# Kernel optimization log

Measured on AMD Instinct MI355X. Metric: run time of the kernel, lower is better.

## Reference

```python
import jax, jax.numpy as jnp
import numpy as np

B, N, E, FIMG = 8, 10242, 61440, 512


def setup_inputs() -> dict:
    key = jax.random.key(0)
    ks = jax.random.split(key, 16)
    inp = {
        "batch_vertices": jax.random.normal(ks[0], (B, N, 3), jnp.float32),
        "img_features": jax.random.normal(ks[1], (B, FIMG), jnp.float32),
        "edge_indices": jax.random.randint(ks[2], (2, E), 0, N, dtype=jnp.int32),
    }
    dims = [(3 + FIMG, 512), (512, 512), (512, 512), (512, 512), (512, 64), (64, 3)]
    for i, (fi, fo) in enumerate(dims, 1):
        inp[f"W{i}"] = jax.random.normal(ks[2 + i], (fi, fo), jnp.float32) / np.sqrt(fi).astype(np.float32)
        inp[f"b{i}"] = jnp.zeros((fo,), jnp.float32)
    return inp


def _gcn(x, W, b, src, dst, norm, n):
    # GCNConv: h = x @ W ; out[i] = sum_{(j->i)} norm_e * h[j] ; + b
    h = jnp.einsum('bnf,fo->bno', x, W)
    msg = h[:, src, :] * norm[None, :, None]        # [B, E+N, Fo]
    out = jnp.zeros((x.shape[0], n, W.shape[1]), x.dtype).at[:, dst, :].add(msg)
    return out + b


def reference(batch_vertices, img_features, edge_indices,
              W1, b1, W2, b2, W3, b3, W4, b4, W5, b5, W6, b6):
    n = batch_vertices.shape[1]
    loop = jnp.arange(n, dtype=edge_indices.dtype)
    src = jnp.concatenate([edge_indices[0], loop])  # add self-loops (GCN)
    dst = jnp.concatenate([edge_indices[1], loop])
    deg = jnp.zeros((n,), jnp.float32).at[dst].add(1.0)
    dinv = jnp.where(deg > 0, jax.lax.rsqrt(deg), 0.0)
    norm = dinv[src] * dinv[dst]                    # symmetric normalization

    feat = jnp.broadcast_to(img_features[:, None, :], (batch_vertices.shape[0], n, img_features.shape[1]))
    x = jnp.concatenate([batch_vertices, feat], axis=2)

    x = _gcn(x, W1, b1, src, dst, norm, n)
    x = _gcn(x, W2, b2, src, dst, norm, n)
    x = jax.nn.relu(x)
    x = _gcn(x, W3, b3, src, dst, norm, n)
    x = _gcn(x, W4, b4, src, dst, norm, n)
    x = jax.nn.relu(x)
    x = _gcn(x, W5, b5, src, dst, norm, n)
    x = _gcn(x, W6, b6, src, dst, norm, n)
    return x
```

## Files before the change

kernel.cpp:

```cpp
#include <hip/hip_runtime.h>
#include <hip/hip_bf16.h>

typedef __attribute__((ext_vector_type(8))) short short8_t;
typedef __attribute__((ext_vector_type(4))) float f32x4;

#define DEV __device__ __forceinline__

constexpr int BB = 8;
constexpr int NV = 10242;
constexpr int NE = 61440;
constexpr int MROWS = BB * NV;
constexpr int KD = 512;

DEV float bf2f(ushort u) { union { unsigned i; float f; } v; v.i = ((unsigned)u) << 16; return v.f; }
DEV ushort f2bf(float f) {
    union { unsigned i; float f; } v; v.f = f;
    unsigned b = v.i;
    b += 0x7fffu + ((b >> 16) & 1u);
    return (ushort)(b >> 16);
}

__global__ void k_init(int* deg, int* fill) {
    int i = blockIdx.x * 256 + threadIdx.x;
    if (i < NV) { deg[i] = 1; fill[i] = 0; }
}

__global__ void k_count(const int* __restrict__ ei, int* __restrict__ deg) {
    int e = blockIdx.x * 256 + threadIdx.x;
    if (e < NE) atomicAdd(&deg[ei[NE + e]], 1);
}

__global__ __launch_bounds__(1024) void k_scan(const int* __restrict__ cnt, int* __restrict__ rp) {
    __shared__ int part[1024];
    const int t = threadIdx.x;
    const int chunk = (NV + 1023) / 1024;
    int b0 = t * chunk, b1 = min(b0 + chunk, NV);
    int s = 0;
    for (int i = b0; i < b1; ++i) s += cnt[i];
    part[t] = s;
    __syncthreads();
    for (int off = 1; off < 1024; off <<= 1) {
        int v = (t >= off) ? part[t - off] : 0;
        __syncthreads();
        part[t] += v;
        __syncthreads();
    }
    int run = (t == 0) ? 0 : part[t - 1];
    for (int i = b0; i < b1; ++i) { rp[i] = run; run += cnt[i]; }
    if (t == 1023) rp[NV] = part[1023];
}

__global__ void k_fill(const int* __restrict__ ei, const int* __restrict__ rp,
                       int* __restrict__ fill, const int* __restrict__ deg,
                       int* __restrict__ ci, float* __restrict__ val) {
    int e = blockIdx.x * 256 + threadIdx.x;
    if (e >= NE + NV) return;
    int s, d;
    if (e < NE) { s = ei[e]; d = ei[NE + e]; }
    else        { s = d = e - NE; }
    int p = atomicAdd(&fill[d], 1);
    int pos = rp[d] + p;
    ci[pos] = s;
    val[pos] = rsqrtf((float)deg[s]) * rsqrtf((float)deg[d]);
}

__global__ void k_srow(const int* __restrict__ rp, const float* __restrict__ val, float* __restrict__ s) {
    int i = blockIdx.x * 256 + threadIdx.x;
    if (i >= NV) return;
    float a = 0.f;
    for (int e = rp[i]; e < rp[i + 1]; ++e) a += val[e];
    s[i] = a;
}

__global__ void k_s2(const int* __restrict__ rp, const int* __restrict__ ci,
                     const float* __restrict__ val, const float* __restrict__ s, float* __restrict__ s2) {
    int i = blockIdx.x * 256 + threadIdx.x;
    if (i >= NV) return;
    float a = 0.f;
    for (int e = rp[i]; e < rp[i + 1]; ++e) a += val[e] * s[ci[e]];
    s2[i] = a;
}

__global__ __launch_bounds__(256) void k_aggsm(const float* __restrict__ src, float* __restrict__ dst,
                                               const int* __restrict__ rp, const int* __restrict__ ci,
                                               const float* __restrict__ val) {
    int idx = blockIdx.x * 256 + threadIdx.x;
    if (idx >= MROWS) return;
    int b = idx / NV, i = idx - b * NV;
    float a0 = 0.f, a1 = 0.f, a2 = 0.f;
    const float* sb = src + (size_t)b * NV * 3;
    for (int e = rp[i]; e < rp[i + 1]; ++e) {
        int j = ci[e];
        float wv = val[e];
        a0 = fmaf(wv, sb[j * 3 + 0], a0);
        a1 = fmaf(wv, sb[j * 3 + 1], a1);
        a2 = fmaf(wv, sb[j * 3 + 2], a2);
    }
    float* o = dst + ((size_t)b * NV + i) * 3;
    o[0] = a0; o[1] = a1; o[2] = a2;
}

__global__ void k_wprep(const float* __restrict__ W4, const float* __restrict__ W3,
                        const float* __restrict__ W5, ushort* __restrict__ Wt4,
                        ushort* __restrict__ W3c, ushort* __restrict__ Wt5) {
    int idx = blockIdx.x * 256 + threadIdx.x;
    if (idx < 512 * 512) {
        int n = idx >> 9, k = idx & 511;
        Wt4[idx] = f2bf(W4[k * 512 + n]);
    } else if (idx < 2 * 512 * 512) {
        int j = idx - 512 * 512;
        W3c[j] = f2bf(W3[j]);
    } else {
        int j = idx - 2 * 512 * 512;
        if (j < 64 * 512) {
            int n = j >> 9, k = j & 511;
            Wt5[j] = f2bf(W5[k * 64 + n]);
        }
    }
}

__global__ __launch_bounds__(128) void k_small1(const float* __restrict__ W1, const float* __restrict__ b1,
                                                const float* __restrict__ b3, const float* __restrict__ W2,
                                                const float* __restrict__ W4, float* __restrict__ CW12,
                                                float* __restrict__ b1w2, float* __restrict__ b3w4) {
    int c = blockIdx.x * 128 + threadIdx.x;
    int y = blockIdx.y;
    const float* Mrow = (y < 3) ? (W1 + y * 512) : (y == 3 ? b1 : b3);
    const float* W = (y < 4) ? W2 : W4;
    float a = 0.f;
    for (int k = 0; k < 512; ++k) a = fmaf(Mrow[k], W[(size_t)k * 512 + c], a);
    float* o = (y < 3) ? (CW12 + y * 512) : (y == 3 ? b1w2 : b3w4);
    o[c] = a;
}

__global__ __launch_bounds__(128) void k_l1base(const float* __restrict__ img, const float* __restrict__ W1,
                                                float* __restrict__ base) {
    int c = blockIdx.x * 128 + threadIdx.x;
    int b = blockIdx.y;
    float s = 0.f;
    for (int k = 0; k < 512; ++k) s = fmaf(img[b * 512 + k], W1[(size_t)(3 + k) * 512 + c], s);
    base[b * 512 + c] = s;
}

__global__ __launch_bounds__(128) void k_matvecs(const float* __restrict__ M, const float* __restrict__ W,
                                                 float* __restrict__ out) {
    int c = blockIdx.x * 128 + threadIdx.x;
    int r = blockIdx.y;
    float a = 0.f;
    for (int k = 0; k < 512; ++k) a = fmaf(M[r * 512 + k], W[(size_t)k * 512 + c], a);
    out[r * 512 + c] = a;
}

__global__ __launch_bounds__(256) void k_x2(const float* __restrict__ aggV2, const float* __restrict__ s,
                                            const float* __restrict__ s2, const float* __restrict__ CW12,
                                            const float* __restrict__ bw2, const float* __restrict__ b1w2,
                                            const float* __restrict__ b2, ushort* __restrict__ r2) {
    const int t = threadIdx.x;
    int row = blockIdx.x * 2 + (t >> 7);
    if (row >= MROWS) return;
    int i = row >> 3, b = row & 7;
    const float* av = aggV2 + ((size_t)b * NV + i) * 3;
    float a0 = av[0], a1 = av[1], a2 = av[2];
    float si = s[i], s2i = s2[i];
    int c = (t & 127) * 4;
    float4 w0 = *(const float4*)&CW12[c];
    float4 w1 = *(const float4*)&CW12[512 + c];
    float4 w2 = *(const float4*)&CW12[1024 + c];
    float4 bw = *(const float4*)&bw2[b * 512 + c];
    float4 bv = *(const float4*)&b1w2[c];
    float4 b2v = *(const float4*)&b2[c];
    float o0 = a0 * w0.x + a1 * w1.x + a2 * w2.x + s2i * bw.x + si * bv.x + b2v.x;
    float o1 = a0 * w0.y + a1 * w1.y + a2 * w2.y + s2i * bw.y + si * bv.y + b2v.y;
    float o2 = a0 * w0.z + a1 * w1.z + a2 * w2.z + s2i * bw.z + si * bv.z + b2v.z;
    float o3 = a0 * w0.w + a1 * w1.w + a2 * w2.w + s2i * bw.w + si * bv.w + b2v.w;
    ushort4 o;
    o.x = f2bf(fmaxf(o0, 0.f));
    o.y = f2bf(fmaxf(o1, 0.f));
    o.z = f2bf(fmaxf(o2, 0.f));
    o.w = f2bf(fmaxf(o3, 0.f));
    *(ushort4*)&r2[(size_t)row * 512 + c] = o;
}

template <int EPI>
__global__ __launch_bounds__(256) void k_gemm(const ushort* __restrict__ A, const ushort* __restrict__ Bt,
                                              ushort* __restrict__ C, int Mr, int Nc,
                                              const float* __restrict__ sv, const float* __restrict__ eb1,
                                              const float* __restrict__ eb2) {
    const int ncb = (Nc + 127) >> 7;
    const int nrc = (Mr + 127) >> 7;
    const int cpx = (nrc + 7) >> 3;
    const int bid = blockIdx.x;
    const int xcd = bid & 7;
    const int k = bid >> 3;
    const int rc = xcd * cpx + k / ncb;
    const int cb = k % ncb;
    if (rc >= nrc) return;

    __shared__ __align__(16) ushort lA[2][4096];
    __shared__ __align__(16) ushort lB[2][4096];
    const int t = threadIdx.x;
    const int lane = t & 63, w = t >> 6;
    const int wr = w >> 1, wc = w & 1;
    const int r0 = rc * 128, c0 = cb * 128;

    const ushort* gA[2]; const ushort* gB[2];
    int ldsoff[2];
    #pragma unroll
    for (int i2 = 0; i2 < 2; ++i2) {
        int idx = i2 * 256 + t;
        int row = idx >> 2, slot = idx & 3;
        int srcslot = slot ^ ((row >> 1) & 3);
        int ar = min(r0 + row, Mr - 1);
        int bc = min(c0 + row, Nc - 1);
        gA[i2] = A + (size_t)ar * KD + srcslot * 8;
        gB[i2] = Bt + (size_t)bc * KD + srcslot * 8;
        ldsoff[i2] = idx * 8;
    }

    auto stage = [&](int buf, int kt) {
        int ko = kt * 32;
        #pragma unroll
        for (int i2 = 0; i2 < 2; ++i2) {
            __builtin_amdgcn_global_load_lds(
                (const __attribute__((address_space(1))) void*)(gA[i2] + ko),
                (__attribute__((address_space(3))) void*)(&lA[buf][ldsoff[i2]]), 16, 0, 0);
            __builtin_amdgcn_global_load_lds(
                (const __attribute__((address_space(1))) void*)(gB[i2] + ko),
                (__attribute__((address_space(3))) void*)(&lB[buf][ldsoff[i2]]), 16, 0, 0);
        }
    };

    f32x4 acc[4][4] = {};
    stage(0, 0);
    __syncthreads();
    int cur = 0;
    const int rloc = lane & 15;
    const int kb = lane >> 4;
    const int kbs = (kb ^ ((rloc >> 1) & 3)) * 8;
    for (int kt = 0; kt < 16; ++kt) {
        if (kt < 15) stage(cur ^ 1, kt + 1);
        short8_t af[4], bfr[4];
        #pragma unroll
        for (int m = 0; m < 4; ++m) {
            af[m]  = *(const short8_t*)&lA[cur][(wr * 64 + m * 16 + rloc) * 32 + kbs];
            bfr[m] = *(const short8_t*)&lB[cur][(wc * 64 + m * 16 + rloc) * 32 + kbs];
        }
        #pragma unroll
        for (int m = 0; m < 4; ++m)
            #pragma unroll
            for (int n = 0; n < 4; ++n)
                acc[m][n] = __builtin_amdgcn_mfma_f32_16x16x32_bf16(bfr[n], af[m], acc[m][n], 0, 0, 0);
        __syncthreads();
        cur ^= 1;
    }

    #pragma unroll
    for (int m = 0; m < 4; ++m) {
        const int gr = r0 + wr * 64 + m * 16 + rloc;
        if (gr >= Mr) continue;
        #pragma unroll
        for (int n = 0; n < 4; ++n) {
            const int qc = c0 + wc * 64 + n * 16;
            if (qc >= Nc) continue;
            const int gc = qc + kb * 4;
            float v0 = acc[m][n][0], v1 = acc[m][n][1], v2 = acc[m][n][2], v3 = acc[m][n][3];
            if (EPI == 1) {
                const float s = sv[gr >> 3];
                const float4 e1 = *(const float4*)&eb1[gc];
                const float4 e2 = *(const float4*)&eb2[gc];
                v0 = fmaxf(v0 + s * e1.x + e2.x, 0.f);
                v1 = fmaxf(v1 + s * e1.y + e2.y, 0.f);
                v2 = fmaxf(v2 + s * e1.z + e2.z, 0.f);
                v3 = fmaxf(v3 + s * e1.w + e2.w, 0.f);
            }
            ushort4 o;
            o.x = f2bf(v0); o.y = f2bf(v1); o.z = f2bf(v2); o.w = f2bf(v3);
            *(ushort4*)&C[(size_t)gr * Nc + gc] = o;
        }
    }
}

__global__ __launch_bounds__(256) void k_gemm64(const ushort* __restrict__ A, const ushort* __restrict__ Bt,
                                                ushort* __restrict__ C) {
    const int rc = blockIdx.x;
    const int r0 = rc * 256;
    __shared__ __align__(16) ushort lA[2][8192];
    __shared__ __align__(16) ushort lB[2][2048];
    const int t = threadIdx.x;
    const int lane = t & 63, w = t >> 6;

    const ushort* gA[4]; int loffA[4];
    #pragma unroll
    for (int p = 0; p < 4; ++p) {
        int idx = p * 256 + t;
        int row = idx >> 2, slot = idx & 3;
        int srcslot = slot ^ ((row >> 1) & 3);
        int ar = min(r0 + row, MROWS - 1);
        gA[p] = A + (size_t)ar * KD + srcslot * 8;
        loffA[p] = idx * 8;
    }
    const int brow = t >> 2, bslot = (t & 3) ^ ((brow >> 1) & 3);
    const ushort* gB = Bt + (size_t)brow * KD + bslot * 8;
    const int loffB = t * 8;

    auto stage = [&](int buf, int kt) {
        int ko = kt * 32;
        #pragma unroll
        for (int p = 0; p < 4; ++p)
            __builtin_amdgcn_global_load_lds(
                (const __attribute__((address_space(1))) void*)(gA[p] + ko),
                (__attribute__((address_space(3))) void*)(&lA[buf][loffA[p]]), 16, 0, 0);
        __builtin_amdgcn_global_load_lds(
            (const __attribute__((address_space(1))) void*)(gB + ko),
            (__attribute__((address_space(3))) void*)(&lB[buf][loffB]), 16, 0, 0);
    };

    f32x4 acc[4][4] = {};
    stage(0, 0);
    __syncthreads();
    int cur = 0;
    const int rloc = lane & 15;
    const int kb = lane >> 4;
    const int kbs = (kb ^ ((rloc >> 1) & 3)) * 8;
    for (int kt = 0; kt < 16; ++kt) {
        if (kt < 15) stage(cur ^ 1, kt + 1);
        short8_t af[4], bfr[4];
        #pragma unroll
        for (int m = 0; m < 4; ++m) {
            af[m]  = *(const short8_t*)&lA[cur][(w * 64 + m * 16 + rloc) * 32 + kbs];
            bfr[m] = *(const short8_t*)&lB[cur][(m * 16 + rloc) * 32 + kbs];
        }
        #pragma unroll
        for (int m = 0; m < 4; ++m)
            #pragma unroll
            for (int n = 0; n < 4; ++n)
                acc[m][n] = __builtin_amdgcn_mfma_f32_16x16x32_bf16(bfr[n], af[m], acc[m][n], 0, 0, 0);
        __syncthreads();
        cur ^= 1;
    }

    #pragma unroll
    for (int m = 0; m < 4; ++m) {
        const int gr = r0 + w * 64 + m * 16 + rloc;
        if (gr >= MROWS) continue;
        #pragma unroll
        for (int n = 0; n < 4; ++n) {
            const int gc = n * 16 + kb * 4;
            ushort4 o;
            o.x = f2bf(acc[m][n][0]); o.y = f2bf(acc[m][n][1]);
            o.z = f2bf(acc[m][n][2]); o.w = f2bf(acc[m][n][3]);
            *(ushort4*)&C[(size_t)gr * 64 + gc] = o;
        }
    }
}

template <bool RELU>
__global__ __launch_bounds__(512) void k_aggv(const ushort* __restrict__ h, ushort* __restrict__ xo,
                                              const int* __restrict__ rp, const int* __restrict__ ci,
                                              const float* __restrict__ val) {
    constexpr int CH = BB * 512;
    const int i = blockIdx.x;
    const int t = threadIdx.x;
    const int r0 = rp[i], r1 = rp[i + 1];
    const ushort* hb = h + t * 8;
    float acc[8] = {};
    for (int e = r0; e < r1; e += 4) {
        const bool p1 = e + 1 < r1, p2 = e + 2 < r1, p3 = e + 3 < r1;
        const int j0 = ci[e];
        const int j1 = p1 ? ci[e + 1] : j0;
        const int j2 = p2 ? ci[e + 2] : j0;
        const int j3 = p3 ? ci[e + 3] : j0;
        const float w0 = val[e];
        const float w1 = p1 ? val[e + 1] : 0.f;
        const float w2 = p2 ? val[e + 2] : 0.f;
        const float w3 = p3 ? val[e + 3] : 0.f;
        const short8_t v0 = *(const short8_t*)(hb + (size_t)j0 * CH);
        const short8_t v1 = *(const short8_t*)(hb + (size_t)j1 * CH);
        const short8_t v2 = *(const short8_t*)(hb + (size_t)j2 * CH);
        const short8_t v3 = *(const short8_t*)(hb + (size_t)j3 * CH);
        #pragma unroll
        for (int k = 0; k < 8; ++k) {
            float a = acc[k];
            a = fmaf(w0, bf2f((ushort)v0[k]), a);
            a = fmaf(w1, bf2f((ushort)v1[k]), a);
            a = fmaf(w2, bf2f((ushort)v2[k]), a);
            a = fmaf(w3, bf2f((ushort)v3[k]), a);
            acc[k] = a;
        }
    }
    short8_t o;
    #pragma unroll
    for (int k = 0; k < 8; ++k) {
        float a = acc[k];
        if (RELU) a = fmaxf(a, 0.f);
        o[k] = (short)f2bf(a);
    }
    *(short8_t*)(xo + (size_t)i * CH + t * 8) = o;
}

__global__ __launch_bounds__(64) void k_aggv64f(const ushort* __restrict__ h, float* __restrict__ h3,
                                                const int* __restrict__ rp, const int* __restrict__ ci,
                                                const float* __restrict__ val, const float* __restrict__ b5,
                                                const float* __restrict__ W6) {
    constexpr int CH = BB * 64;
    __shared__ float w6[192];
    const int t = threadIdx.x;
    w6[t] = W6[t]; w6[t + 64] = W6[t + 64]; w6[t + 128] = W6[t + 128];
    __syncthreads();
    const int i = blockIdx.x;
    const int r0 = rp[i], r1 = rp[i + 1];
    const ushort* hb = h + t * 8;
    float acc[8] = {};
    for (int e = r0; e < r1; e += 4) {
        const bool p1 = e + 1 < r1, p2 = e + 2 < r1, p3 = e + 3 < r1;
        const int j0 = ci[e];
        const int j1 = p1 ? ci[e + 1] : j0;
        const int j2 = p2 ? ci[e + 2] : j0;
        const int j3 = p3 ? ci[e + 3] : j0;
        const float w0 = val[e];
        const float w1 = p1 ? val[e + 1] : 0.f;
        const float w2 = p2 ? val[e + 2] : 0.f;
        const float w3 = p3 ? val[e + 3] : 0.f;
        const short8_t v0 = *(const short8_t*)(hb + (size_t)j0 * CH);
        const short8_t v1 = *(const short8_t*)(hb + (size_t)j1 * CH);
        const short8_t v2 = *(const short8_t*)(hb + (size_t)j2 * CH);
        const short8_t v3 = *(const short8_t*)(hb + (size_t)j3 * CH);
        #pragma unroll
        for (int k = 0; k < 8; ++k) {
            float a = acc[k];
            a = fmaf(w0, bf2f((ushort)v0[k]), a);
            a = fmaf(w1, bf2f((ushort)v1[k]), a);
            a = fmaf(w2, bf2f((ushort)v2[k]), a);
            a = fmaf(w3, bf2f((ushort)v3[k]), a);
            acc[k] = a;
        }
    }
    const int fb = (t & 7) * 8;
    float p0 = 0.f, p1 = 0.f, p2 = 0.f;
    #pragma unroll
    for (int k = 0; k < 8; ++k) {
        float a = acc[k] + b5[fb + k];
        p0 = fmaf(a, w6[(fb + k) * 3 + 0], p0);
        p1 = fmaf(a, w6[(fb + k) * 3 + 1], p1);
        p2 = fmaf(a, w6[(fb + k) * 3 + 2], p2);
    }
    p0 += __shfl_xor(p0, 1); p0 += __shfl_xor(p0, 2); p0 += __shfl_xor(p0, 4);
    p1 += __shfl_xor(p1, 1); p1 += __shfl_xor(p1, 2); p1 += __shfl_xor(p1, 4);
    p2 += __shfl_xor(p2, 1); p2 += __shfl_xor(p2, 2); p2 += __shfl_xor(p2, 4);
    if ((t & 7) == 0) {
        int row = i * 8 + (t >> 3);
        float* o = h3 + (size_t)row * 3;
        o[0] = p0; o[1] = p1; o[2] = p2;
    }
}

__global__ __launch_bounds__(256) void k_agg3(const float* __restrict__ h3, float* __restrict__ out,
                                              const int* __restrict__ rp, const int* __restrict__ ci,
                                              const float* __restrict__ val, const float* __restrict__ b6) {
    int idx = blockIdx.x * 256 + threadIdx.x;
    if (idx >= MROWS) return;
    int b = idx / NV, i = idx - b * NV;
    float a0 = b6[0], a1 = b6[1], a2 = b6[2];
    int r0 = rp[i], r1 = rp[i + 1];
    for (int e = r0; e < r1; ++e) {
        int j = ci[e];
        float wv = val[e];
        const float* hr = h3 + ((size_t)j * BB + b) * 3;
        a0 = fmaf(wv, hr[0], a0);
        a1 = fmaf(wv, hr[1], a1);
        a2 = fmaf(wv, hr[2], a2);
    }
    float* o = out + (size_t)idx * 3;
    o[0] = a0; o[1] = a1; o[2] = a2;
}

extern "C" void kernel_launch(void* const* d_in, const int* in_sizes, int n_in,
                              void* d_out, int out_size, void* d_ws, size_t ws_size,
                              hipStream_t stream) {
    const float* verts = (const float*)d_in[0];
    const float* img   = (const float*)d_in[1];
    const int*   ei    = (const int*)d_in[2];
    const float* W1 = (const float*)d_in[3];  const float* b1 = (const float*)d_in[4];
    const float* W2 = (const float*)d_in[5];  const float* b2 = (const float*)d_in[6];
    const float* W3 = (const float*)d_in[7];  const float* b3 = (const float*)d_in[8];
    const float* W4 = (const float*)d_in[9];  const float* b4 = (const float*)d_in[10];
    const float* W5 = (const float*)d_in[11]; const float* b5 = (const float*)d_in[12];
    const float* W6 = (const float*)d_in[13]; const float* b6 = (const float*)d_in[14];
    float* out = (float*)d_out;

    char* ws = (char*)d_ws;
    size_t off = 0;
    auto carve = [&](size_t bytes) -> void* {
        void* q = ws + off;
        off += (bytes + 255) & ~(size_t)255;
        return q;
    };
    ushort* bufA = (ushort*)carve((size_t)MROWS * 512 * 2);
    ushort* bufB = (ushort*)carve((size_t)MROWS * 512 * 2);
    ushort* Wt4  = (ushort*)carve((size_t)512 * 512 * 2);
    ushort* W3c  = (ushort*)carve((size_t)512 * 512 * 2);
    ushort* Wt34 = (ushort*)carve((size_t)512 * 512 * 2);
    ushort* Wt5  = (ushort*)carve((size_t)64 * 512 * 2);
    float*  basev = (float*)carve((size_t)BB * 512 * 4);
    float*  bw2   = (float*)carve((size_t)BB * 512 * 4);
    float*  CW12  = (float*)carve((size_t)3 * 512 * 4);
    float*  b1w2  = (float*)carve((size_t)512 * 4);
    float*  b3w4  = (float*)carve((size_t)512 * 4);
    int*    deg  = (int*)carve((size_t)NV * 4);
    int*    fill = (int*)carve((size_t)NV * 4);
    float*  sV   = (float*)carve((size_t)NV * 4);
    float*  s2V  = (float*)carve((size_t)NV * 4);
    int*    rp   = (int*)carve((size_t)(NV + 1) * 4);
    int*    ci   = (int*)carve((size_t)(NE + NV) * 4);
    float*  valv = (float*)carve((size_t)(NE + NV) * 4);
    float*  aggV  = (float*)carve((size_t)MROWS * 3 * 4);
    float*  aggV2 = (float*)carve((size_t)MROWS * 3 * 4);
    float*  h3   = (float*)carve((size_t)MROWS * 3 * 4);

    dim3 b256(256);
    const int gNV = (NV + 255) / 256;
    const int gMR = (MROWS + 255) / 256;
    k_init<<<dim3(gNV), b256, 0, stream>>>(deg, fill);
    k_count<<<dim3((NE + 255) / 256), b256, 0, stream>>>(ei, deg);
    k_scan<<<dim3(1), dim3(1024), 0, stream>>>(deg, rp);
    k_fill<<<dim3((NE + NV + 255) / 256), b256, 0, stream>>>(ei, rp, fill, deg, ci, valv);
    k_srow<<<dim3(gNV), b256, 0, stream>>>(rp, valv, sV);
    k_s2<<<dim3(gNV), b256, 0, stream>>>(rp, ci, valv, sV, s2V);
    k_aggsm<<<dim3(gMR), b256, 0, stream>>>(verts, aggV, rp, ci, valv);
    k_aggsm<<<dim3(gMR), b256, 0, stream>>>(aggV, aggV2, rp, ci, valv);
    k_wprep<<<dim3((2 * 512 * 512 + 64 * 512 + 255) / 256), b256, 0, stream>>>(W4, W3, W5, Wt4, W3c, Wt5);
    k_small1<<<dim3(4, 5), dim3(128), 0, stream>>>(W1, b1, b3, W2, W4, CW12, b1w2, b3w4);
    k_l1base<<<dim3(4, BB), dim3(128), 0, stream>>>(img, W1, basev);
    k_matvecs<<<dim3(4, BB), dim3(128), 0, stream>>>(basev, W2, bw2);
    k_gemm<0><<<dim3(32), b256, 0, stream>>>(Wt4, W3c, Wt34, 512, 512, nullptr, nullptr, nullptr);
    k_x2<<<dim3((MROWS + 1) / 2), b256, 0, stream>>>(aggV2, sV, s2V, CW12, bw2, b1w2, b2, bufA);
    k_aggv<false><<<dim3(NV), dim3(512), 0, stream>>>(bufA, bufB, rp, ci, valv);
    k_aggv<false><<<dim3(NV), dim3(512), 0, stream>>>(bufB, bufA, rp, ci, valv);
    const int nrc = (MROWS + 127) / 128;
    const int g512 = 8 * ((nrc + 7) / 8) * 4;
    k_gemm<1><<<dim3(g512), b256, 0, stream>>>(bufA, Wt34, bufB, MROWS, 512, sV, b3w4, b4);
    k_gemm64<<<dim3((MROWS + 255) / 256), b256, 0, stream>>>(bufB, Wt5, bufA);
    k_aggv64f<<<dim3(NV), dim3(64), 0, stream>>>(bufA, h3, rp, ci, valv, b5, W6);
    k_agg3<<<dim3(gMR), b256, 0, stream>>>(h3, out, rp, ci, valv, b6);
}
```

Baseline: 477.0 us.

## Merge small setup kernels and triple-buffer GEMM LDS staging with vmcnt waits

Several small preprocessing kernels are merged into fewer launches: row-sum and second-order row-sum ride along with the 3-wide aggregation, and weight conversion plus the small matvecs are combined into one prep kernel. Separately, the main bf16 GEMM moves from double to triple buffering of LDS tiles, prefetching two K-steps ahead and using explicit vmcnt waits with raw barriers instead of __syncthreads. This aims to cut launch overhead and hide global-load latency in the GEMM, at the cost of more LDS per block (possibly lower occupancy) and reliance on the compiler issuing loads in the order the vmcnt counts assume.

```diff
diff --git a/kernel.cpp b/kernel.cpp
--- a/kernel.cpp
+++ b/kernel.cpp
@@ -64,82 +64,79 @@
     val[pos] = rsqrtf((float)deg[s]) * rsqrtf((float)deg[d]);
 }
 
-__global__ void k_srow(const int* __restrict__ rp, const float* __restrict__ val, float* __restrict__ s) {
-    int i = blockIdx.x * 256 + threadIdx.x;
-    if (i >= NV) return;
-    float a = 0.f;
-    for (int e = rp[i]; e < rp[i + 1]; ++e) a += val[e];
-    s[i] = a;
-}
-
-__global__ void k_s2(const int* __restrict__ rp, const int* __restrict__ ci,
-                     const float* __restrict__ val, const float* __restrict__ s, float* __restrict__ s2) {
-    int i = blockIdx.x * 256 + threadIdx.x;
-    if (i >= NV) return;
-    float a = 0.f;
-    for (int e = rp[i]; e < rp[i + 1]; ++e) a += val[e] * s[ci[e]];
-    s2[i] = a;
-}
-
-__global__ __launch_bounds__(256) void k_aggsm(const float* __restrict__ src, float* __restrict__ dst,
+__global__ __launch_bounds__(256) void k_aggsc(const float* __restrict__ src, float* __restrict__ dst,
                                                const int* __restrict__ rp, const int* __restrict__ ci,
-                                               const float* __restrict__ val) {
-    int idx = blockIdx.x * 256 + threadIdx.x;
-    if (idx >= MROWS) return;
-    int b = idx / NV, i = idx - b * NV;
-    float a0 = 0.f, a1 = 0.f, a2 = 0.f;
-    const float* sb = src + (size_t)b * NV * 3;
-    for (int e = rp[i]; e < rp[i + 1]; ++e) {
-        int j = ci[e];
-        float wv = val[e];
-        a0 = fmaf(wv, sb[j * 3 + 0], a0);
-        a1 = fmaf(wv, sb[j * 3 + 1], a1);
-        a2 = fmaf(wv, sb[j * 3 + 2], a2);
-    }
-    float* o = dst + ((size_t)b * NV + i) * 3;
-    o[0] = a0; o[1] = a1; o[2] = a2;
-}
-
-__global__ void k_wprep(const float* __restrict__ W4, const float* __restrict__ W3,
-                        const float* __restrict__ W5, ushort* __restrict__ Wt4,
-                        ushort* __restrict__ W3c, ushort* __restrict__ Wt5) {
-    int idx = blockIdx.x * 256 + threadIdx.x;
-    if (idx < 512 * 512) {
-        int n = idx >> 9, k = idx & 511;
-        Wt4[idx] = f2bf(W4[k * 512 + n]);
-    } else if (idx < 2 * 512 * 512) {
-        int j = idx - 512 * 512;
-        W3c[j] = f2bf(W3[j]);
+                                               const float* __restrict__ val,
+                                               const float* __restrict__ sin, float* __restrict__ sout,
+                                               int gMR_) {
+    const int bid = blockIdx.x;
+    if (bid < gMR_) {
+        int idx = bid * 256 + threadIdx.x;
+        if (idx >= MROWS) return;
+        int b = idx / NV, i = idx - b * NV;
+        float a0 = 0.f, a1 = 0.f, a2 = 0.f;
+        const float* sb = src + (size_t)b * NV * 3;
+        for (int e = rp[i]; e < rp[i + 1]; ++e) {
+            int j = ci[e];
+            float wv = val[e];
+            a0 = fmaf(wv, sb[j * 3 + 0], a0);
+            a1 = fmaf(wv, sb[j * 3 + 1], a1);
+            a2 = fmaf(wv, sb[j * 3 + 2], a2);
+        }
+        float* o = dst + ((size_t)b * NV + i) * 3;
+        o[0] = a0; o[1] = a1; o[2] = a2;
     } else {
-        int j = idx - 2 * 512 * 512;
-        if (j < 64 * 512) {
+        int i = (bid - gMR_) * 256 + threadIdx.x;
+        if (i >= NV) return;
+        float a = 0.f;
+        if (sin) { for (int e = rp[i]; e < rp[i + 1]; ++e) a = fmaf(val[e], sin[ci[e]], a); }
+        else     { for (int e = rp[i]; e < rp[i + 1]; ++e) a += val[e]; }
+        sout[i] = a;
+    }
+}
+
+__global__ __launch_bounds__(256) void k_prep(const float* __restrict__ W4, const float* __restrict__ W3,
+                                              const float* __restrict__ W5, const float* __restrict__ W1,
+                                              const float* __restrict__ b1, const float* __restrict__ b3,
+                                              const float* __restrict__ W2, const float* __restrict__ img,
+                                              ushort* __restrict__ Wt4, ushort* __restrict__ W3c,
+                                              ushort* __restrict__ Wt5, float* __restrict__ CW12,
+                                              float* __restrict__ b1w2, float* __restrict__ b3w4,
+                                              float* __restrict__ basev) {
+    constexpr int WB = (2 * 512 * 512 + 64 * 512) / 256;
+    const int bid = blockIdx.x;
+    const int t = threadIdx.x;
+    if (bid < WB) {
+        int idx = bid * 256 + t;
+        if (idx < 512 * 512) {
+            int n = idx >> 9, k = idx & 511;
+            Wt4[idx] = f2bf(W4[k * 512 + n]);
+        } else if (idx < 2 * 512 * 512) {
+            int j = idx - 512 * 512;
+            W3c[j] = f2bf(W3[j]);
+        } else {
+            int j = idx - 2 * 512 * 512;
             int n = j >> 9, k = j & 511;
             Wt5[j] = f2bf(W5[k * 64 + n]);
         }
-    }
-}
-
-__global__ __launch_bounds__(128) void k_small1(const float* __restrict__ W1, const float* __restrict__ b1,
-                                                const float* __restrict__ b3, const float* __restrict__ W2,
-                                                const float* __restrict__ W4, float* __restrict__ CW12,
-                                                float* __restrict__ b1w2, float* __restrict__ b3w4) {
-    int c = blockIdx.x * 128 + threadIdx.x;
-    int y = blockIdx.y;
-    const float* Mrow = (y < 3) ? (W1 + y * 512) : (y == 3 ? b1 : b3);
-    const float* W = (y < 4) ? W2 : W4;
-    float a = 0.f;
-    for (int k = 0; k < 512; ++k) a = fmaf(Mrow[k], W[(size_t)k * 512 + c], a);
-    float* o = (y < 3) ? (CW12 + y * 512) : (y == 3 ? b1w2 : b3w4);
-    o[c] = a;
-}
-
-__global__ __launch_bounds__(128) void k_l1base(const float* __restrict__ img, const float* __restrict__ W1,
-                                                float* __restrict__ base) {
-    int c = blockIdx.x * 128 + threadIdx.x;
-    int b = blockIdx.y;
-    float s = 0.f;
-    for (int k = 0; k < 512; ++k) s = fmaf(img[b * 512 + k], W1[(size_t)(3 + k) * 512 + c], s);
-    base[b * 512 + c] = s;
+    } else if (bid < WB + 10) {
+        int r = bid - WB;
+        int y = r >> 1;
+        int c = (r & 1) * 256 + t;
+        const float* Mrow = (y < 3) ? (W1 + y * 512) : (y == 3 ? b1 : b3);
+        const float* W = (y < 4) ? W2 : W4;
+        float a = 0.f;
+        for (int k = 0; k < 512; ++k) a = fmaf(Mrow[k], W[(size_t)k * 512 + c], a);
+        float* o = (y < 3) ? (CW12 + y * 512) : (y == 3 ? b1w2 : b3w4);
+        o[c] = a;
+    } else {
+        int r = bid - (WB + 10);
+        int b = r >> 1;
+        int c = (r & 1) * 256 + t;
+        float s = 0.f;
+        for (int k = 0; k < 512; ++k) s = fmaf(img[b * 512 + k], W1[(size_t)(3 + k) * 512 + c], s);
+        basev[b * 512 + c] = s;
+    }
 }
 
 __global__ __launch_bounds__(128) void k_matvecs(const float* __restrict__ M, const float* __restrict__ W,
@@ -181,6 +178,13 @@
     *(ushort4*)&r2[(size_t)row * 512 + c] = o;
 }
 
+#define WAITVM(n) do { \
+    asm volatile("s_waitcnt vmcnt(" #n ")" ::: "memory"); \
+    __builtin_amdgcn_sched_barrier(0); \
+    __builtin_amdgcn_s_barrier(); \
+    __builtin_amdgcn_sched_barrier(0); \
+} while (0)
+
 template <int EPI>
 __global__ __launch_bounds__(256) void k_gemm(const ushort* __restrict__ A, const ushort* __restrict__ Bt,
                                               ushort* __restrict__ C, int Mr, int Nc,
@@ -196,8 +200,8 @@
     const int cb = k % ncb;
     if (rc >= nrc) return;
 
-    __shared__ __align__(16) ushort lA[2][4096];
-    __shared__ __align__(16) ushort lB[2][4096];
+    __shared__ __align__(16) ushort lA[3][4096];
+    __shared__ __align__(16) ushort lB[3][4096];
     const int t = threadIdx.x;
     const int lane = t & 63, w = t >> 6;
     const int wr = w >> 1, wc = w & 1;
@@ -231,28 +235,39 @@
     };
 
     f32x4 acc[4][4] = {};
-    stage(0, 0);
-    __syncthreads();
-    int cur = 0;
     const int rloc = lane & 15;
     const int kb = lane >> 4;
     const int kbs = (kb ^ ((rloc >> 1) & 3)) * 8;
-    for (int kt = 0; kt < 16; ++kt) {
-        if (kt < 15) stage(cur ^ 1, kt + 1);
+
+    auto compute = [&](int buf) {
         short8_t af[4], bfr[4];
         #pragma unroll
         for (int m = 0; m < 4; ++m) {
-            af[m]  = *(const short8_t*)&lA[cur][(wr * 64 + m * 16 + rloc) * 32 + kbs];
-            bfr[m] = *(const short8_t*)&lB[cur][(wc * 64 + m * 16 + rloc) * 32 + kbs];
+            af[m]  = *(const short8_t*)&lA[buf][(wr * 64 + m * 16 + rloc) * 32 + kbs];
+            bfr[m] = *(const short8_t*)&lB[buf][(wc * 64 + m * 16 + rloc) * 32 + kbs];
         }
         #pragma unroll
         for (int m = 0; m < 4; ++m)
             #pragma unroll
             for (int n = 0; n < 4; ++n)
                 acc[m][n] = __builtin_amdgcn_mfma_f32_16x16x32_bf16(bfr[n], af[m], acc[m][n], 0, 0, 0);
-        __syncthreads();
-        cur ^= 1;
-    }
+    };
+
+    stage(0, 0);
+    stage(1, 1);
+    WAITVM(4);
+    int cur = 0;
+    for (int kt = 0; kt < 14; ++kt) {
+        int sb = cur + 2; if (sb > 2) sb -= 3;
+        stage(sb, kt + 2);
+        compute(cur);
+        WAITVM(4);
+        cur = (cur == 2) ? 0 : cur + 1;
+    }
+    compute(cur);
+    WAITVM(0);
+    cur = (cur == 2) ? 0 : cur + 1;
+    compute(cur);
 
     #pragma unroll
     for (int m = 0; m < 4; ++m) {
@@ -524,13 +539,10 @@
     k_count<<<dim3((NE + 255) / 256), b256, 0, stream>>>(ei, deg);
     k_scan<<<dim3(1), dim3(1024), 0, stream>>>(deg, rp);
     k_fill<<<dim3((NE + NV + 255) / 256), b256, 0, stream>>>(ei, rp, fill, deg, ci, valv);
-    k_srow<<<dim3(gNV), b256, 0, stream>>>(rp, valv, sV);
-    k_s2<<<dim3(gNV), b256, 0, stream>>>(rp, ci, valv, sV, s2V);
-    k_aggsm<<<dim3(gMR), b256, 0, stream>>>(verts, aggV, rp, ci, valv);
-    k_aggsm<<<dim3(gMR), b256, 0, stream>>>(aggV, aggV2, rp, ci, valv);
-    k_wprep<<<dim3((2 * 512 * 512 + 64 * 512 + 255) / 256), b256, 0, stream>>>(W4, W3, W5, Wt4, W3c, Wt5);
-    k_small1<<<dim3(4, 5), dim3(128), 0, stream>>>(W1, b1, b3, W2, W4, CW12, b1w2, b3w4);
-    k_l1base<<<dim3(4, BB), dim3(128), 0, stream>>>(img, W1, basev);
+    k_aggsc<<<dim3(gMR + gNV), b256, 0, stream>>>(verts, aggV, rp, ci, valv, nullptr, sV, gMR);
+    k_aggsc<<<dim3(gMR + gNV), b256, 0, stream>>>(aggV, aggV2, rp, ci, valv, sV, s2V, gMR);
+    k_prep<<<dim3(2176 + 10 + 16), b256, 0, stream>>>(W4, W3, W5, W1, b1, b3, W2, img,
+                                                      Wt4, W3c, Wt5, CW12, b1w2, b3w4, basev);
     k_matvecs<<<dim3(4, BB), dim3(128), 0, stream>>>(basev, W2, bw2);
     k_gemm<0><<<dim3(32), b256, 0, stream>>>(Wt4, W3c, Wt34, 512, 512, nullptr, nullptr, nullptr);
     k_x2<<<dim3((MROWS + 1) / 2), b256, 0, stream>>>(aggV2, sV, s2V, CW12, bw2, b1w2, b2, bufA);
```

Measured after the change: 455.2 us. 4.6% less time.
